# Kernel optimization log

Hardware: AMD Instinct MI355X
Metric: run time of the kernel (lower is better)

The kernel has to match this reference:

```python
import jax, jax.numpy as jnp
import numpy as np

B, N1, N2, DEG = 64, 512, 512, 16
NF, NH, NL = 128, 128, 3
RATIO = 0.5
K1 = int(np.ceil(RATIO * N1))
K2 = int(np.ceil(RATIO * N2))
NCLS = 2
NCAT = NH * NL  # 384


def _gl(key, shape, fan_in):
    return jax.random.normal(key, shape, jnp.float32) / np.sqrt(fan_in)


def setup_inputs() -> dict:
    key = jax.random.key(0)
    ks = jax.random.split(key, 24)
    x = jax.random.normal(ks[0], (B * (N1 + N2), NF), jnp.float32)
    # edges within each component of each graph (c1-local / c2-local and global indexing)
    s1 = jax.random.randint(ks[1], (B, N1 * DEG), 0, N1)
    d1 = jax.random.randint(ks[2], (B, N1 * DEG), 0, N1)
    s2 = jax.random.randint(ks[3], (B, N2 * DEG), 0, N2)
    d2 = jax.random.randint(ks[4], (B, N2 * DEG), 0, N2)
    off1 = (jnp.arange(B) * N1)[:, None]
    off2 = (jnp.arange(B) * N2)[:, None]
    offg = (jnp.arange(B) * (N1 + N2))[:, None]
    src_c1 = (s1 + off1).reshape(-1).astype(jnp.int32)
    dst_c1 = (d1 + off1).reshape(-1).astype(jnp.int32)
    src_c2 = (s2 + off2).reshape(-1).astype(jnp.int32)
    dst_c2 = (d2 + off2).reshape(-1).astype(jnp.int32)
    src_all = jnp.concatenate([(s1 + offg).reshape(-1), (s2 + N1 + offg).reshape(-1)]).astype(jnp.int32)
    dst_all = jnp.concatenate([(d1 + offg).reshape(-1), (d2 + N1 + offg).reshape(-1)]).astype(jnp.int32)
    return {
        'x': x,
        'src_all': src_all, 'dst_all': dst_all,
        'src_c1': src_c1, 'dst_c1': dst_c1,
        'src_c2': src_c2, 'dst_c2': dst_c2,
        'W1': _gl(ks[5], (NF, NH), NF), 'b1': jnp.zeros((NH,), jnp.float32),
        'W2': _gl(ks[6], (NH, NH), NH), 'b2': jnp.zeros((NH,), jnp.float32),
        'W3': _gl(ks[7], (NH, NH), NH), 'b3': jnp.zeros((NH,), jnp.float32),
        'Wg_att': _gl(ks[8], (NCAT, NCAT), NCAT),
        'Wal': _gl(ks[9], (2 * NCAT, 2 * NCAT), 2 * NCAT), 'bal': jnp.zeros((2 * NCAT,), jnp.float32),
        'Wf': _gl(ks[10], (NCAT, NH), NCAT), 'bf': jnp.zeros((NH,), jnp.float32),
        'Wg_fin': _gl(ks[11], (NH, NH), NH),
        'Wl1': _gl(ks[12], (2 * NH, NH), 2 * NH), 'bl1': jnp.zeros((NH,), jnp.float32),
        'Wl2': _gl(ks[13], (NH, NH // 2), NH), 'bl2': jnp.zeros((NH // 2,), jnp.float32),
        'Wl3': _gl(ks[14], (NH // 2, NCLS), NH // 2), 'bl3': jnp.zeros((NCLS,), jnp.float32),
    }


def gcn_conv(x, src, dst, emask, W, b, n):
    # PyG GCNConv: symmetric norm with self-loops; masked edges contribute zero.
    xw = x @ W
    w = emask.astype(x.dtype)
    src_s = jnp.where(emask, src, 0)
    dst_s = jnp.where(emask, dst, 0)
    deg = jax.ops.segment_sum(w, dst_s, num_segments=n) + 1.0  # +1 self-loop
    dis = jax.lax.rsqrt(deg)
    norm = dis[src_s] * dis[dst_s] * w
    out = jax.ops.segment_sum(xw[src_s] * norm[:, None], dst_s, num_segments=n)
    out = out + xw * (dis * dis)[:, None]  # self-loop message
    return out + b


def att_pool(x, batch, counts, Wg, nseg):
    # global_pool with cfg 'ATT': gap -> tanh(W) -> broadcast -> sigmoid gate -> sum pool
    mean = jax.ops.segment_sum(x, batch, num_segments=nseg) / counts[:, None]
    c = jnp.tanh(mean @ Wg)
    alpha = jax.nn.sigmoid(jnp.sum(x * c[batch], axis=1, keepdims=True))
    return jax.ops.segment_sum(x * alpha, batch, num_segments=nseg)


def cag_pool(xc, src, dst, pv, n_per, k):
    # CAGPool_layer: score = <x, pool_vec>/||pool_vec||, per-graph topk, gate by sigmoid(score)
    batch = jnp.repeat(jnp.arange(B), n_per)
    x_ = pv[batch]
    score = jnp.sum(xc * x_, axis=1) / jnp.linalg.norm(x_, axis=1)
    order = jnp.argsort(-score.reshape(B, n_per), axis=1)[:, :k]
    perm = (order + (jnp.arange(B) * n_per)[:, None]).reshape(-1)  # [B*k]
    pooled = xc[perm] * jax.nn.sigmoid(score[perm])[:, None]
    # filter_adj: remap kept nodes, mask out edges touching dropped nodes
    node_map = jnp.full((B * n_per,), -1, dtype=jnp.int32).at[perm].set(jnp.arange(B * k, dtype=jnp.int32))
    r, c = node_map[src], node_map[dst]
    emask = (r >= 0) & (c >= 0)
    return pooled, r, c, emask


def reference(x, src_all, dst_all, src_c1, dst_c1, src_c2, dst_c2,
              W1, b1, W2, b2, W3, b3, Wg_att, Wal, bal, Wf, bf, Wg_fin,
              Wl1, bl1, Wl2, bl2, Wl3, bl3):
    N = B * (N1 + N2)
    ones_all = jnp.ones(src_all.shape[0], dtype=bool)
    h = jax.nn.relu(gcn_conv(x, src_all, dst_all, ones_all, W1, b1, N))
    xs = [h]
    for W, b in ((W2, b2), (W3, b3)):
        h = jax.nn.relu(gcn_conv(h, src_all, dst_all, ones_all, W, b, N))
        xs.append(h)
    xcat = jnp.concatenate(xs, axis=1)  # [N, NCAT]
    # split combined node set into c1 / c2 components (static layout)
    offg = (jnp.arange(B) * (N1 + N2))[:, None]
    idx1 = (offg + jnp.arange(N1)[None, :]).reshape(-1)
    idx2 = (offg + N1 + jnp.arange(N2)[None, :]).reshape(-1)
    x_c1, x_c2 = xcat[idx1], xcat[idx2]
    batch_c1 = jnp.repeat(jnp.arange(B), N1)
    batch_c2 = jnp.repeat(jnp.arange(B), N2)
    x12 = jnp.concatenate([x_c1, x_c2], axis=0)
    batch_ = jnp.concatenate([batch_c1, batch_c2 + B])
    counts = jnp.concatenate([jnp.full((B,), N1, jnp.float32), jnp.full((B,), N2, jnp.float32)])
    gp = att_pool(x12, batch_, counts, Wg_att, 2 * B)
    pv = jnp.concatenate([gp[:B], gp[B:]], axis=1) @ Wal + bal  # att_lin
    pv1, pv2 = pv[:, :NCAT], pv[:, NCAT:]
    p1, r1, c1e, m1 = cag_pool(x_c1, src_c1, dst_c1, pv1, N1, K1)
    p2, r2, c2e, m2 = cag_pool(x_c2, src_c2, dst_c2, pv2, N2, K2)
    h1 = jax.nn.relu(gcn_conv(p1, r1, c1e, m1, Wf, bf, B * K1))
    h2 = jax.nn.relu(gcn_conv(p2, r2, c2e, m2, Wf, bf, B * K2))
    g1 = att_pool(h1, jnp.repeat(jnp.arange(B), K1), jnp.full((B,), K1, jnp.float32), Wg_fin, B)
    g2 = att_pool(h2, jnp.repeat(jnp.arange(B), K2), jnp.full((B,), K2, jnp.float32), Wg_fin, B)
    pred = jnp.concatenate([g1, g2], axis=1)
    pred = jax.nn.relu(pred @ Wl1 + bl1)
    pred = jax.nn.relu(pred @ Wl2 + bl2)
    return pred @ Wl3 + bl3  # [B, NCLS]
```

## Files before the change

kernel.cpp:

```cpp
#include <hip/hip_runtime.h>
#include <math.h>

constexpr int BB   = 64;
constexpr int NPB  = 1024;
constexpr int NN   = BB * NPB;
constexpr int EALL = 1048576;
constexpr int EC   = 524288;
constexpr int EPG  = 8192;
constexpr int KTOP = 256;
constexpr int NP   = BB * KTOP;
constexpr int NP2  = 2 * NP;

typedef __attribute__((ext_vector_type(8))) short bf16x8;
typedef __attribute__((ext_vector_type(4))) unsigned short us4;
typedef __attribute__((ext_vector_type(8))) unsigned short us8;
typedef __attribute__((ext_vector_type(4))) float f32x4;

__device__ __forceinline__ unsigned short f2bf(float f) {
    return (unsigned short)(__float_as_uint(f) >> 16);
}
__device__ __forceinline__ float bf2f(unsigned short h) {
    return __uint_as_float(((unsigned)h) << 16);
}

__device__ __forceinline__ int pq(int q) { return q ^ (q >> 3); }

__global__ __launch_bounds__(256) void k_build_csr(const int* __restrict__ src_all,
                                                   const int* __restrict__ dst_all,
                                                   int* __restrict__ rowstart,
                                                   int* __restrict__ csrc,
                                                   float* __restrict__ dis) {
    __shared__ int cnt[512];
    __shared__ int rs[512];
    __shared__ int wsum[4];
    __shared__ int stage[EPG];
    const int g = blockIdx.x;
    const int b = g >> 1, c = g & 1;
    const int ebase  = c * EC + b * EPG;
    const int region = g * EPG;
    const int nbase  = g * 512;
    const int t = threadIdx.x;
    const int lane = t & 63, w = t >> 6;

    cnt[t] = 0; cnt[t + 256] = 0;
    __syncthreads();
    for (int i = 0; i < 32; i++) {
        int d = dst_all[ebase + t + 256 * i] & 511;
        atomicAdd(&cnt[d], 1);
    }
    __syncthreads();
    int v0 = cnt[2 * t], v1 = cnt[2 * t + 1];
    int p = v0 + v1;
    int incl = p;
    for (int off = 1; off < 64; off <<= 1) {
        int u = __shfl_up(incl, off);
        if (lane >= off) incl += u;
    }
    if (lane == 63) wsum[w] = incl;
    __syncthreads();
    int base = 0;
    for (int i = 0; i < w; i++) base += wsum[i];
    int excl = base + incl - p;
    rs[2 * t] = excl;
    rs[2 * t + 1] = excl + v0;
    rowstart[nbase + 2 * t]     = region + excl;
    rowstart[nbase + 2 * t + 1] = region + excl + v0;
    dis[nbase + 2 * t]     = 1.0f / sqrtf((float)v0 + 1.0f);
    dis[nbase + 2 * t + 1] = 1.0f / sqrtf((float)v1 + 1.0f);
    if (g == 127 && t == 0) rowstart[NN] = EALL;
    __syncthreads();
    for (int i = 0; i < 32; i++) {
        int e = ebase + t + 256 * i;
        int d = dst_all[e] & 511;
        int pp = atomicAdd(&rs[d], 1);
        stage[pp] = src_all[e];
    }
    __syncthreads();
    for (int i = 0; i < 32; i++)
        csrc[region + t + 256 * i] = stage[t + 256 * i];
}

__global__ __launch_bounds__(256) void k_build_csr_pooled(const int* __restrict__ s1,
                                                          const int* __restrict__ d1,
                                                          const int* __restrict__ s2,
                                                          const int* __restrict__ d2,
                                                          const int* __restrict__ nmap,
                                                          int* __restrict__ rowstart,
                                                          int* __restrict__ cntp,
                                                          int* __restrict__ csre,
                                                          float* __restrict__ disp) {
    __shared__ int cnt[256];
    __shared__ int rs[256];
    __shared__ int wsum[4];
    __shared__ int stage[EPG];
    const int g = blockIdx.x;
    const int c = g >> 6, b = g & 63;
    const int* ss = c ? s2 : s1;
    const int* dd = c ? d2 : d1;
    const int* nm = nmap + c * 32768;
    const int ebase  = b * EPG;
    const int region = g * EPG;
    const int nbase  = g * 256;
    const int t = threadIdx.x;
    const int lane = t & 63, w = t >> 6;

    cnt[t] = 0;
    __syncthreads();
    for (int i = 0; i < 32; i++) {
        int e = ebase + t + 256 * i;
        int r = nm[ss[e]], cc = nm[dd[e]];
        if (r >= 0 && cc >= 0) atomicAdd(&cnt[cc & 255], 1);
    }
    __syncthreads();
    int v = cnt[t];
    int incl = v;
    for (int off = 1; off < 64; off <<= 1) {
        int u = __shfl_up(incl, off);
        if (lane >= off) incl += u;
    }
    if (lane == 63) wsum[w] = incl;
    __syncthreads();
    int base = 0;
    for (int i = 0; i < w; i++) base += wsum[i];
    int excl = base + incl - v;
    rs[t] = excl;
    rowstart[nbase + t] = region + excl;
    cntp[nbase + t] = v;
    disp[nbase + t] = 1.0f / sqrtf((float)v + 1.0f);
    __syncthreads();
    for (int i = 0; i < 32; i++) {
        int e = ebase + t + 256 * i;
        int r = nm[ss[e]], cc = nm[dd[e]];
        if (r >= 0 && cc >= 0) {
            int pp = atomicAdd(&rs[cc & 255], 1);
            stage[pp] = r;
        }
    }
    __syncthreads();
    for (int i = 0; i < 32; i++)
        csre[region + t + 256 * i] = stage[t + 256 * i];
}

template <int KDIM>
__global__ __launch_bounds__(256) void k_gemm_tile(const float* __restrict__ A, int lda,
                                                   const float* __restrict__ W,
                                                   const float* __restrict__ rowscale,
                                                   float* __restrict__ C, int M) {
    __shared__ float As[32][132];
    __shared__ float Ws[32 * 128];
    const int tid  = threadIdx.x;
    const int c0 = (tid & 15) * 8;
    const int r0 = (tid >> 4) * 8;
    const int row0 = blockIdx.x * 128;
    const int arow = tid >> 1;
    const int aq   = tid & 1;
    const float* Ap = A + (size_t)(row0 + arow) * lda;
    const int pq0 = pq(c0 >> 2) * 4;
    const int pq1 = pq((c0 >> 2) + 1) * 4;

    float acc[8][8];
#pragma unroll
    for (int i = 0; i < 8; i++)
#pragma unroll
        for (int j = 0; j < 8; j++) acc[i][j] = 0.f;

    float4 areg[4], wreg[4];
#pragma unroll
    for (int qq = 0; qq < 4; qq++)
        areg[qq] = *(const float4*)(Ap + (aq + 2 * qq) * 4);
#pragma unroll
    for (int q = 0; q < 4; q++) {
        int f = tid + 256 * q;
        wreg[q] = *(const float4*)(W + (size_t)(f >> 5) * 128 + (f & 31) * 4);
    }

    constexpr int NT = KDIM / 32;
    for (int t = 0; t < NT; t++) {
#pragma unroll
        for (int qq = 0; qq < 4; qq++) {
            int kk = (aq + 2 * qq) * 4;
            As[kk + 0][arow] = areg[qq].x;
            As[kk + 1][arow] = areg[qq].y;
            As[kk + 2][arow] = areg[qq].z;
            As[kk + 3][arow] = areg[qq].w;
        }
#pragma unroll
        for (int q = 0; q < 4; q++) {
            int f = tid + 256 * q;
            *(float4*)&Ws[(f >> 5) * 128 + pq(f & 31) * 4] = wreg[q];
        }
        __syncthreads();
        if (t + 1 < NT) {
            int k0 = (t + 1) * 32;
#pragma unroll
            for (int qq = 0; qq < 4; qq++)
                areg[qq] = *(const float4*)(Ap + k0 + (aq + 2 * qq) * 4);
#pragma unroll
            for (int q = 0; q < 4; q++) {
                int f = tid + 256 * q;
                wreg[q] = *(const float4*)(W + (size_t)(k0 + (f >> 5)) * 128 + (f & 31) * 4);
            }
        }
#pragma unroll 2
        for (int kk = 0; kk < 32; kk++) {
            float4 a0 = *(const float4*)&As[kk][r0];
            float4 a1 = *(const float4*)&As[kk][r0 + 4];
            float4 b0 = *(const float4*)&Ws[kk * 128 + pq0];
            float4 b1 = *(const float4*)&Ws[kk * 128 + pq1];
            float a[8] = {a0.x, a0.y, a0.z, a0.w, a1.x, a1.y, a1.z, a1.w};
            float b[8] = {b0.x, b0.y, b0.z, b0.w, b1.x, b1.y, b1.z, b1.w};
#pragma unroll
            for (int i = 0; i < 8; i++)
#pragma unroll
                for (int j = 0; j < 8; j++)
                    acc[i][j] = fmaf(a[i], b[j], acc[i][j]);
        }
        if (t + 1 < NT) __syncthreads();
    }
#pragma unroll
    for (int i = 0; i < 8; i++) {
        int row = row0 + r0 + i;
        if (row < M) {
            float sc = rowscale[row];
            float4 o0 = {acc[i][0]*sc, acc[i][1]*sc, acc[i][2]*sc, acc[i][3]*sc};
            float4 o1 = {acc[i][4]*sc, acc[i][5]*sc, acc[i][6]*sc, acc[i][7]*sc};
            *(float4*)(C + (size_t)row * 128 + c0) = o0;
            *(float4*)(C + (size_t)row * 128 + c0 + 4) = o1;
        }
    }
}

__global__ void k_prep_wf(const float* __restrict__ Wf,
                          unsigned short* __restrict__ hi, unsigned short* __restrict__ lo) {
    int g = blockIdx.x * 256 + threadIdx.x;
    int n = g / 384, k = g - n * 384;
    float v = Wf[k * 128 + n];
    unsigned short h = f2bf(v);
    hi[g] = h;
    lo[g] = f2bf(v - bf2f(h));
}

__global__ __launch_bounds__(256) void k_gemm_gather_mfma(const float* __restrict__ XC,
                                                          const int* __restrict__ sel,
                                                          const float* __restrict__ SC,
                                                          const float* __restrict__ rowscale,
                                                          const unsigned short* __restrict__ WH,
                                                          const unsigned short* __restrict__ WL,
                                                          float* __restrict__ C) {
    __shared__ unsigned short Ah[128][40], Al[128][40], Wh[128][40], Wl[128][40];
    const int tid  = threadIdx.x;
    const int wid  = tid >> 6, lane = tid & 63;
    const int quad = lane >> 4, m15 = lane & 15;
    const int row0 = blockIdx.x * 128;
    const int arow = tid >> 1, aq = tid & 1;
    const int wn   = tid >> 1, wh2 = tid & 1;

    int n = row0 + arow;
    int comm = n >= NP;
    int nl = n - (comm ? NP : 0);
    int b = nl >> 8;
    int old = sel[n];
    const float* Ap = XC + (size_t)(b * NPB + comm * 512 + old) * 384;
    float scv = SC[comm * 32768 + b * 512 + old];
    float sg = 1.f / (1.f + expf(-scv));

    f32x4 acc[2][8];
#pragma unroll
    for (int i = 0; i < 2; i++)
#pragma unroll
        for (int j = 0; j < 8; j++) acc[i][j] = (f32x4){0.f, 0.f, 0.f, 0.f};

    float4 areg[4];
#pragma unroll
    for (int qq = 0; qq < 4; qq++)
        areg[qq] = *(const float4*)(Ap + (aq + 2 * qq) * 4);

    constexpr int NT = 12;
    for (int t = 0; t < NT; t++) {
        if (t) __syncthreads();
#pragma unroll
        for (int qq = 0; qq < 4; qq++) {
            int k = (aq + 2 * qq) * 4;
            float4 v = areg[qq];
            v.x *= sg; v.y *= sg; v.z *= sg; v.w *= sg;
            us4 h, l;
            h.x = f2bf(v.x); l.x = f2bf(v.x - bf2f(h.x));
            h.y = f2bf(v.y); l.y = f2bf(v.y - bf2f(h.y));
            h.z = f2bf(v.z); l.z = f2bf(v.z - bf2f(h.z));
            h.w = f2bf(v.w); l.w = f2bf(v.w - bf2f(h.w));
            *(us4*)&Ah[arow][k] = h;
            *(us4*)&Al[arow][k] = l;
        }
        int k0 = t * 32;
#pragma unroll
        for (int c = 0; c < 2; c++) {
            int kc = 8 * (wh2 + 2 * c);
            *(us8*)&Wh[wn][kc] = *(const us8*)&WH[(size_t)wn * 384 + k0 + kc];
            *(us8*)&Wl[wn][kc] = *(const us8*)&WL[(size_t)wn * 384 + k0 + kc];
        }
        __syncthreads();
        if (t + 1 < NT) {
            int kn = (t + 1) * 32;
#pragma unroll
            for (int qq = 0; qq < 4; qq++)
                areg[qq] = *(const float4*)(Ap + kn + (aq + 2 * qq) * 4);
        }
        bf16x8 ah[2], al2[2];
#pragma unroll
        for (int rt = 0; rt < 2; rt++) {
            int r = wid * 32 + rt * 16 + m15;
            ah[rt]  = *(const bf16x8*)&Ah[r][quad * 8];
            al2[rt] = *(const bf16x8*)&Al[r][quad * 8];
        }
#pragma unroll
        for (int ct = 0; ct < 8; ct++) {
            int nn = ct * 16 + m15;
            bf16x8 bh = *(const bf16x8*)&Wh[nn][quad * 8];
            bf16x8 bl = *(const bf16x8*)&Wl[nn][quad * 8];
#pragma unroll
            for (int rt = 0; rt < 2; rt++) {
                acc[rt][ct] = __builtin_amdgcn_mfma_f32_16x16x32_bf16(ah[rt], bh, acc[rt][ct], 0, 0, 0);
                acc[rt][ct] = __builtin_amdgcn_mfma_f32_16x16x32_bf16(al2[rt], bh, acc[rt][ct], 0, 0, 0);
                acc[rt][ct] = __builtin_amdgcn_mfma_f32_16x16x32_bf16(ah[rt], bl, acc[rt][ct], 0, 0, 0);
            }
        }
    }
#pragma unroll
    for (int rt = 0; rt < 2; rt++)
#pragma unroll
        for (int reg = 0; reg < 4; reg++) {
            int row = row0 + wid * 32 + rt * 16 + quad * 4 + reg;
            float sc = rowscale[row];
#pragma unroll
            for (int ct = 0; ct < 8; ct++)
                C[(size_t)row * 128 + ct * 16 + m15] = acc[rt][ct][reg] * sc;
        }
}

__global__ void k_aggregate4(const float* __restrict__ xwsc, const float* __restrict__ dis,
                             const int* __restrict__ rowstart, const int* __restrict__ csrc,
                             const float* __restrict__ bias, float* __restrict__ XC, int colbase,
                             float* __restrict__ mpart) {
    __shared__ float redf[8][128];
    int xcd  = blockIdx.x & 7;
    int slot = blockIdx.x >> 3;
    int g    = ((slot >> 6) << 3) | xcd;
    int bslot = slot & 63;
    int node = g * 512 + bslot * 8 + (threadIdx.x >> 5);
    int l    = threadIdx.x & 31;
    const float4* xw4 = (const float4*)xwsc;
    float4 acc = xw4[(size_t)node * 32 + l];
    int e0 = rowstart[node], e1 = rowstart[node + 1];
    int e = e0;
    for (; e + 4 <= e1; e += 4) {
        int s0 = csrc[e], s1 = csrc[e + 1], s2 = csrc[e + 2], s3 = csrc[e + 3];
        float4 u0 = xw4[(size_t)s0 * 32 + l];
        float4 u1 = xw4[(size_t)s1 * 32 + l];
        float4 u2 = xw4[(size_t)s2 * 32 + l];
        float4 u3 = xw4[(size_t)s3 * 32 + l];
        acc.x += (u0.x + u1.x) + (u2.x + u3.x);
        acc.y += (u0.y + u1.y) + (u2.y + u3.y);
        acc.z += (u0.z + u1.z) + (u2.z + u3.z);
        acc.w += (u0.w + u1.w) + (u2.w + u3.w);
    }
    for (; e < e1; e++) {
        int s = csrc[e];
        float4 u = xw4[(size_t)s * 32 + l];
        acc.x += u.x; acc.y += u.y; acc.z += u.z; acc.w += u.w;
    }
    float di = dis[node];
    float4 b4 = ((const float4*)bias)[l];
    acc.x = fmaxf(acc.x * di + b4.x, 0.f);
    acc.y = fmaxf(acc.y * di + b4.y, 0.f);
    acc.z = fmaxf(acc.z * di + b4.z, 0.f);
    acc.w = fmaxf(acc.w * di + b4.w, 0.f);
    *(float4*)(XC + (size_t)node * 384 + colbase + l * 4) = acc;
    *(float4*)&redf[threadIdx.x >> 5][l * 4] = acc;
    __syncthreads();
    if (threadIdx.x < 128) {
        int c = threadIdx.x;
        float s = 0.f;
#pragma unroll
        for (int r = 0; r < 8; r++) s += redf[r][c];
        mpart[((size_t)(g * 64 + bslot)) * 384 + colbase + c] = s;
    }
}

__global__ void k_aggregate_pooled(const float* __restrict__ xw, const float* __restrict__ disp,
                                   const int* __restrict__ rowstart, const int* __restrict__ cntp,
                                   const int* __restrict__ csre,
                                   const float* __restrict__ bias, float* __restrict__ H,
                                   float* __restrict__ meansum) {
    __shared__ float redf[8][128];
    int xcd  = blockIdx.x & 7;
    int slot = blockIdx.x >> 3;
    int g    = ((slot >> 5) << 3) | xcd;
    int node = g * 256 + (slot & 31) * 8 + (threadIdx.x >> 5);
    int l    = threadIdx.x & 31;
    const float4* x4 = (const float4*)xw;
    float4 acc = x4[(size_t)node * 32 + l];
    int e0 = rowstart[node], nE = cntp[node];
    int e = e0, eend = e0 + nE;
    for (; e + 4 <= eend; e += 4) {
        int s0 = csre[e], s1 = csre[e + 1], s2 = csre[e + 2], s3 = csre[e + 3];
        float4 u0 = x4[(size_t)s0 * 32 + l];
        float4 u1 = x4[(size_t)s1 * 32 + l];
        float4 u2 = x4[(size_t)s2 * 32 + l];
        float4 u3 = x4[(size_t)s3 * 32 + l];
        acc.x += (u0.x + u1.x) + (u2.x + u3.x);
        acc.y += (u0.y + u1.y) + (u2.y + u3.y);
        acc.z += (u0.z + u1.z) + (u2.z + u3.z);
        acc.w += (u0.w + u1.w) + (u2.w + u3.w);
    }
    for (; e < eend; e++) {
        int r = csre[e];
        float4 u = x4[(size_t)r * 32 + l];
        acc.x += u.x; acc.y += u.y; acc.z += u.z; acc.w += u.w;
    }
    float di = disp[node];
    float4 b4 = ((const float4*)bias)[l];
    acc.x = fmaxf(acc.x * di + b4.x, 0.f);
    acc.y = fmaxf(acc.y * di + b4.y, 0.f);
    acc.z = fmaxf(acc.z * di + b4.z, 0.f);
    acc.w = fmaxf(acc.w * di + b4.w, 0.f);
    *(float4*)(H + (size_t)node * 128 + l * 4) = acc;
    *(float4*)&redf[threadIdx.x >> 5][l * 4] = acc;
    __syncthreads();
    if (threadIdx.x < 128) {
        int c = threadIdx.x;
        float s = 0.f;
#pragma unroll
        for (int r = 0; r < 8; r++) s += redf[r][c];
        atomicAdd(&meansum[g * 128 + c], s);
    }
}

__global__ void k_c12(const float* __restrict__ mpart, const float* __restrict__ Wg,
                      float* __restrict__ c12) {
    __shared__ float ms[384];
    int seg = blockIdx.x; int c = threadIdx.x;
    int g = ((seg & 63) << 1) | (seg >> 6);
    float s0 = 0.f;
    for (int s2 = 0; s2 < 64; s2++)
        s0 += mpart[((size_t)(g * 64 + s2)) * 384 + c];
    ms[c] = s0 * (1.0f / 512.0f);
    __syncthreads();
    float s = 0.f;
    for (int k = 0; k < 384; k++) s = fmaf(ms[k], Wg[(size_t)k * 384 + c], s);
    c12[seg * 384 + c] = tanhf(s);
}

__global__ __launch_bounds__(256) void k_attpool1(const float* __restrict__ XC,
                                                  const float* __restrict__ C12,
                                                  float* __restrict__ GPP) {
    __shared__ float gps[4][384];
    int blk = blockIdx.x;
    int gc = blk >> 2, q = blk & 3;
    int seg = ((gc & 1) << 6) | (gc >> 1);
    int w = threadIdx.x >> 6, l = threadIdx.x & 63;
    const float* c12r = C12 + seg * 384;
    float4 cr0 = *(const float4*)(c12r + 4 * l);
    float4 cr1 = (l < 32) ? *(const float4*)(c12r + 256 + 4 * l) : float4{0.f,0.f,0.f,0.f};
    float4 a0 = {0.f,0.f,0.f,0.f}, a1 = {0.f,0.f,0.f,0.f};
    int base = gc * 512 + q * 128 + w * 32;
    for (int it = 0; it < 32; it++) {
        const float* xr = XC + (size_t)(base + it) * 384;
        float4 v0 = *(const float4*)(xr + 4 * l);
        float4 v1 = (l < 32) ? *(const float4*)(xr + 256 + 4 * l) : float4{0.f,0.f,0.f,0.f};
        float s = v0.x*cr0.x + v0.y*cr0.y + v0.z*cr0.z + v0.w*cr0.w
                + v1.x*cr1.x + v1.y*cr1.y + v1.z*cr1.z + v1.w*cr1.w;
        for (int off = 32; off; off >>= 1) s += __shfl_xor(s, off);
        float al = 1.f / (1.f + expf(-s));
        a0.x += v0.x*al; a0.y += v0.y*al; a0.z += v0.z*al; a0.w += v0.w*al;
        a1.x += v1.x*al; a1.y += v1.y*al; a1.z += v1.z*al; a1.w += v1.w*al;
    }
    *(float4*)&gps[w][4 * l] = a0;
    if (l < 32) *(float4*)&gps[w][256 + 4 * l] = a1;
    __syncthreads();
    for (int c = threadIdx.x; c < 384; c += 256) {
        float s = gps[0][c] + gps[1][c] + gps[2][c] + gps[3][c];
        GPP[(size_t)(seg * 4 + q) * 384 + c] = s;
    }
}

__global__ void k_pv(const float* __restrict__ GPP, const float* __restrict__ Wal,
                     const float* __restrict__ bal, float* __restrict__ pv,
                     float* __restrict__ pnorm) {
    __shared__ float gpls[768];
    __shared__ float red[768];
    int row = blockIdx.x;
    int c   = threadIdx.x;
    {
        int seg = (c < 384) ? row : (64 + row);
        int k   = (c < 384) ? c : (c - 384);
        float v = GPP[(size_t)(seg * 4 + 0) * 384 + k] + GPP[(size_t)(seg * 4 + 1) * 384 + k]
                + GPP[(size_t)(seg * 4 + 2) * 384 + k] + GPP[(size_t)(seg * 4 + 3) * 384 + k];
        gpls[c] = v;
    }
    __syncthreads();
    float s = bal[c];
    for (int k = 0; k < 768; k++) s = fmaf(gpls[k], Wal[(size_t)k * 768 + c], s);
    pv[row * 768 + c] = s;
    red[c] = s * s;
    __syncthreads();
    int wv = c >> 6, ln = c & 63;
    if (wv < 2) {
        float s2 = 0.f;
#pragma unroll
        for (int i = 0; i < 6; i++) s2 += red[wv * 384 + ln + 64 * i];
        for (int off = 32; off; off >>= 1) s2 += __shfl_down(s2, off);
        if (ln == 0) pnorm[wv * 64 + row] = sqrtf(s2);
    }
}

__global__ void k_score(const float* __restrict__ XC, const float* __restrict__ pv,
                        const float* __restrict__ pnorm, float* __restrict__ sc) {
    int nl2 = blockIdx.x * 4 + (threadIdx.x >> 6);
    int lane = threadIdx.x & 63;
    int comm = nl2 >> 15;
    int nl = nl2 & 32767;
    int b = nl >> 9; int i = nl & 511;
    const float* xr = XC + (size_t)(b * NPB + comm * 512 + i) * 384;
    const float* pr = pv + b * 768 + comm * 384;
    float4 x0 = *(const float4*)(xr + 4 * lane);
    float4 p0 = *(const float4*)(pr + 4 * lane);
    float s = x0.x*p0.x + x0.y*p0.y + x0.z*p0.z + x0.w*p0.w;
    if (lane < 32) {
        float4 x1 = *(const float4*)(xr + 256 + 4 * lane);
        float4 p1 = *(const float4*)(pr + 256 + 4 * lane);
        s += x1.x*p1.x + x1.y*p1.y + x1.z*p1.z + x1.w*p1.w;
    }
    for (int off = 32; off; off >>= 1) s += __shfl_down(s, off);
    if (lane == 0) sc[comm * 32768 + nl] = s / pnorm[comm * 64 + b];
}

__global__ void k_topk(const float* __restrict__ sc, int* __restrict__ sel, int* __restrict__ nmap) {
    __shared__ float sv[512];
    __shared__ int   si[512];
    int blk = blockIdx.x;
    int t = threadIdx.x;
    sv[t] = sc[blk * 512 + t];             si[t] = t;
    sv[t + 256] = sc[blk * 512 + t + 256]; si[t + 256] = t + 256;
    __syncthreads();
    for (int k2 = 2; k2 <= 512; k2 <<= 1) {
        for (int j = k2 >> 1; j > 0; j >>= 1) {
            for (int i = t; i < 512; i += 256) {
                int l = i ^ j;
                if (l > i) {
                    bool desc = ((i & k2) == 0);
                    float a = sv[i], bb2 = sv[l];
                    bool sw = desc ? (a < bb2) : (a > bb2);
                    if (sw) {
                        sv[i] = bb2; sv[l] = a;
                        int tmp = si[i]; si[i] = si[l]; si[l] = tmp;
                    }
                }
            }
            __syncthreads();
        }
    }
    sel[blk * 256 + t] = si[t];
    nmap[blk * 512 + si[t]] = blk * 256 + t;
    nmap[blk * 512 + si[t + 256]] = -1;
}

__global__ void k_cfin(const float* __restrict__ meansum, const float* __restrict__ Wg,
                       float* __restrict__ cf) {
    __shared__ float ms[128];
    int b = blockIdx.x; int c = threadIdx.x;
    ms[c] = meansum[b * 128 + c] * (1.0f / 256.0f);
    __syncthreads();
    float s = 0.f;
    for (int k = 0; k < 128; k++) s = fmaf(ms[k], Wg[k * 128 + c], s);
    cf[b * 128 + c] = tanhf(s);
}

__global__ __launch_bounds__(256) void k_attpool_fin(const float* __restrict__ H,
                                                     const float* __restrict__ cf,
                                                     float* __restrict__ g12) {
    __shared__ float gps[4][128];
    int seg = blockIdx.x;
    int w = threadIdx.x >> 6, l = threadIdx.x & 63;
    const float2 cfl = *(const float2*)(cf + seg * 128 + 2 * l);
    float2 acc = {0.f, 0.f};
    int base = seg * 256 + w * 64;
    for (int it = 0; it < 64; it++) {
        const float2 h = *(const float2*)(H + (size_t)(base + it) * 128 + 2 * l);
        float s = h.x * cfl.x + h.y * cfl.y;
        for (int off = 32; off; off >>= 1) s += __shfl_xor(s, off);
        float al = 1.f / (1.f + expf(-s));
        acc.x += h.x * al; acc.y += h.y * al;
    }
    *(float2*)&gps[w][2 * l] = acc;
    __syncthreads();
    if (threadIdx.x < 128) {
        int c = threadIdx.x;
        float s = gps[0][c] + gps[1][c] + gps[2][c] + gps[3][c];
        int b = seg & 63, comm = seg >> 6;
        g12[b * 256 + comm * 128 + c] = s;
    }
}

__global__ void k_mlp(const float* __restrict__ G,
                      const float* __restrict__ Wl1, const float* __restrict__ bl1,
                      const float* __restrict__ Wl2, const float* __restrict__ bl2,
                      const float* __restrict__ Wl3, const float* __restrict__ bl3,
                      float* __restrict__ out) {
    __shared__ float t1[128], t2[64];
    int b = blockIdx.x; int t = threadIdx.x;
    float s = bl1[t];
    for (int k = 0; k < 256; k++) s = fmaf(G[b * 256 + k], Wl1[k * 128 + t], s);
    t1[t] = fmaxf(s, 0.f);
    __syncthreads();
    if (t < 64) {
        float s2 = bl2[t];
        for (int k = 0; k < 128; k++) s2 = fmaf(t1[k], Wl2[k * 64 + t], s2);
        t2[t] = fmaxf(s2, 0.f);
    }
    __syncthreads();
    if (t < 2) {
        float s3 = bl3[t];
        for (int k = 0; k < 64; k++) s3 = fmaf(t2[k], Wl3[k * 2 + t], s3);
        out[b * 2 + t] = s3;
    }
}

extern "C" void kernel_launch(void* const* d_in, const int* in_sizes, int n_in,
                              void* d_out, int out_size, void* d_ws, size_t ws_size,
                              hipStream_t stream) {
    const float* x       = (const float*)d_in[0];
    const int*   src_all = (const int*)d_in[1];
    const int*   dst_all = (const int*)d_in[2];
    const int*   src_c1  = (const int*)d_in[3];
    const int*   dst_c1  = (const int*)d_in[4];
    const int*   src_c2  = (const int*)d_in[5];
    const int*   dst_c2  = (const int*)d_in[6];
    const float* W1 = (const float*)d_in[7];   const float* b1 = (const float*)d_in[8];
    const float* W2 = (const float*)d_in[9];   const float* b2 = (const float*)d_in[10];
    const float* W3 = (const float*)d_in[11];  const float* b3 = (const float*)d_in[12];
    const float* Wg_att = (const float*)d_in[13];
    const float* Wal = (const float*)d_in[14]; const float* bal = (const float*)d_in[15];
    const float* Wf  = (const float*)d_in[16]; const float* bf  = (const float*)d_in[17];
    const float* Wg_fin = (const float*)d_in[18];
    const float* Wl1 = (const float*)d_in[19]; const float* bl1 = (const float*)d_in[20];
    const float* Wl2 = (const float*)d_in[21]; const float* bl2 = (const float*)d_in[22];
    const float* Wl3 = (const float*)d_in[23]; const float* bl3 = (const float*)d_in[24];
    float* out = (float*)d_out;

    float* f = (float*)d_ws;
    size_t o = 0;
    float* XC   = f + o; o += (size_t)NN * 384;
    float* SCR  = f + o; o += (size_t)NN * 128;
    float* H    = f + o; o += (size_t)NP2 * 128;
    int* ROWSTART = (int*)(f + o); o += 65552;
    int* CSRC     = (int*)(f + o); o += EALL;
    int* CNTP     = (int*)(f + o); o += NP2;
    float* DIS    = f + o; o += NN;
    float* GPP    = f + o; o += 512 * 384;
    float* MEANF  = f + o; o += 128 * 128;
    float* C12    = f + o; o += 128 * 384;
    float* PV     = f + o; o += 64 * 768;
    float* PNORM  = f + o; o += 128;
    float* SC     = f + o; o += 65536;
    int* SEL      = (int*)(f + o); o += NP2;
    int* NMAP     = (int*)(f + o); o += 65536;
    float* DISP   = f + o; o += NP2;
    float* CFIN   = f + o; o += 128 * 128;
    float* G12    = f + o; o += 64 * 256;
    unsigned short* WBH = (unsigned short*)(f + o); o += 24576;
    unsigned short* WBL = (unsigned short*)(f + o); o += 24576;
    size_t needed_bytes = o * sizeof(float);
    if (ws_size < needed_bytes) return;

    float* MPART = H;
    float* XWP   = SCR;

    hipMemsetAsync(MEANF, 0, 128 * 128 * sizeof(float), stream);

    k_prep_wf<<<192, 256, 0, stream>>>(Wf, WBH, WBL);

    k_build_csr<<<128, 256, 0, stream>>>(src_all, dst_all, ROWSTART, CSRC, DIS);

    k_gemm_tile<128><<<NN / 128, 256, 0, stream>>>(x, 128, W1, DIS, SCR, NN);
    k_aggregate4<<<NN / 8, 256, 0, stream>>>(SCR, DIS, ROWSTART, CSRC, b1, XC, 0, MPART);
    k_gemm_tile<128><<<NN / 128, 256, 0, stream>>>(XC + 0, 384, W2, DIS, SCR, NN);
    k_aggregate4<<<NN / 8, 256, 0, stream>>>(SCR, DIS, ROWSTART, CSRC, b2, XC, 128, MPART);
    k_gemm_tile<128><<<NN / 128, 256, 0, stream>>>(XC + 128, 384, W3, DIS, SCR, NN);
    k_aggregate4<<<NN / 8, 256, 0, stream>>>(SCR, DIS, ROWSTART, CSRC, b3, XC, 256, MPART);

    k_c12<<<128, 384, 0, stream>>>(MPART, Wg_att, C12);
    k_attpool1<<<512, 256, 0, stream>>>(XC, C12, GPP);
    k_pv<<<64, 768, 0, stream>>>(GPP, Wal, bal, PV, PNORM);

    k_score<<<65536 / 4, 256, 0, stream>>>(XC, PV, PNORM, SC);
    k_topk<<<128, 256, 0, stream>>>(SC, SEL, NMAP);

    k_build_csr_pooled<<<128, 256, 0, stream>>>(src_c1, dst_c1, src_c2, dst_c2,
                                                NMAP, ROWSTART, CNTP, CSRC, DISP);

    k_gemm_gather_mfma<<<NP2 / 128, 256, 0, stream>>>(XC, SEL, SC, DISP, WBH, WBL, XWP);
    k_aggregate_pooled<<<NP2 / 8, 256, 0, stream>>>(XWP, DISP, ROWSTART, CNTP, CSRC,
                                                    bf, H, MEANF);

    k_cfin<<<128, 128, 0, stream>>>(MEANF, Wg_fin, CFIN);
    k_attpool_fin<<<128, 256, 0, stream>>>(H, CFIN, G12);

    k_mlp<<<64, 128, 0, stream>>>(G12, Wl1, bl1, Wl2, bl2, Wl3, bl3, out);
}
```

Measured before the change: 575.3 us.

## Replace FP32 SIMT GEMM for GCN layers with split-bf16 MFMA GEMM

```diff
diff --git a/kernel.cpp b/kernel.cpp
--- a/kernel.cpp
+++ b/kernel.cpp
@@ -22,8 +22,6 @@
 __device__ __forceinline__ float bf2f(unsigned short h) {
     return __uint_as_float(((unsigned)h) << 16);
 }
-
-__device__ __forceinline__ int pq(int q) { return q ^ (q >> 3); }
 
 __global__ __launch_bounds__(256) void k_build_csr(const int* __restrict__ src_all,
                                                    const int* __restrict__ dst_all,
@@ -141,103 +139,113 @@
         csre[region + t + 256 * i] = stage[t + 256 * i];
 }
 
+__global__ void k_prep_w(const float* __restrict__ W1, const float* __restrict__ W2,
+                         const float* __restrict__ W3, const float* __restrict__ Wf,
+                         unsigned short* __restrict__ hi, unsigned short* __restrict__ lo) {
+    int g = blockIdx.x * 256 + threadIdx.x;
+    float v; int dst;
+    if (g < 49152) {
+        int mat = g >> 14, rem = g & 16383;
+        int n = rem >> 7, k = rem & 127;
+        const float* W = (mat == 0) ? W1 : (mat == 1) ? W2 : W3;
+        v = W[k * 128 + n];
+        dst = mat * 16384 + n * 128 + k;
+    } else {
+        int rem = g - 49152;
+        int n = rem / 384, k = rem - n * 384;
+        v = Wf[k * 128 + n];
+        dst = 49152 + n * 384 + k;
+    }
+    unsigned short h = f2bf(v);
+    hi[dst] = h;
+    lo[dst] = f2bf(v - bf2f(h));
+}
+
 template <int KDIM>
-__global__ __launch_bounds__(256) void k_gemm_tile(const float* __restrict__ A, int lda,
-                                                   const float* __restrict__ W,
+__global__ __launch_bounds__(256) void k_gemm_mfma(const float* __restrict__ A, int lda,
+                                                   const unsigned short* __restrict__ WH,
+                                                   const unsigned short* __restrict__ WL,
                                                    const float* __restrict__ rowscale,
-                                                   float* __restrict__ C, int M) {
-    __shared__ float As[32][132];
-    __shared__ float Ws[32 * 128];
+                                                   float* __restrict__ C) {
+    __shared__ unsigned short Ah[128][40], Al[128][40], Wh[128][40], Wl[128][40];
     const int tid  = threadIdx.x;
-    const int c0 = (tid & 15) * 8;
-    const int r0 = (tid >> 4) * 8;
+    const int wid  = tid >> 6, lane = tid & 63;
+    const int quad = lane >> 4, m15 = lane & 15;
     const int row0 = blockIdx.x * 128;
-    const int arow = tid >> 1;
-    const int aq   = tid & 1;
+    const int arow = tid >> 1, aq = tid & 1;
+    const int wn   = tid >> 1, wh2 = tid & 1;
     const float* Ap = A + (size_t)(row0 + arow) * lda;
-    const int pq0 = pq(c0 >> 2) * 4;
-    const int pq1 = pq((c0 >> 2) + 1) * 4;
-
-    float acc[8][8];
-#pragma unroll
-    for (int i = 0; i < 8; i++)
-#pragma unroll
-        for (int j = 0; j < 8; j++) acc[i][j] = 0.f;
-
-    float4 areg[4], wreg[4];
+
+    f32x4 acc[2][8];
+#pragma unroll
+    for (int i = 0; i < 2; i++)
+#pragma unroll
+        for (int j = 0; j < 8; j++) acc[i][j] = (f32x4){0.f, 0.f, 0.f, 0.f};
+
+    float4 areg[4];
 #pragma unroll
     for (int qq = 0; qq < 4; qq++)
         areg[qq] = *(const float4*)(Ap + (aq + 2 * qq) * 4);
-#pragma unroll
-    for (int q = 0; q < 4; q++) {
-        int f = tid + 256 * q;
-        wreg[q] = *(const float4*)(W + (size_t)(f >> 5) * 128 + (f & 31) * 4);
-    }
 
     constexpr int NT = KDIM / 32;
     for (int t = 0; t < NT; t++) {
+        if (t) __syncthreads();
 #pragma unroll
         for (int qq = 0; qq < 4; qq++) {
-            int kk = (aq + 2 * qq) * 4;
-            As[kk + 0][arow] = areg[qq].x;
-            As[kk + 1][arow] = areg[qq].y;
-            As[kk + 2][arow] = areg[qq].z;
-            As[kk + 3][arow] = areg[qq].w;
-        }
-#pragma unroll
-        for (int q = 0; q < 4; q++) {
-            int f = tid + 256 * q;
-            *(float4*)&Ws[(f >> 5) * 128 + pq(f & 31) * 4] = wreg[q];
+            int k = (aq + 2 * qq) * 4;
+            float4 v = areg[qq];
+            us4 h, l;
+            h.x = f2bf(v.x); l.x = f2bf(v.x - bf2f(h.x));
+            h.y = f2bf(v.y); l.y = f2bf(v.y - bf2f(h.y));
+            h.z = f2bf(v.z); l.z = f2bf(v.z - bf2f(h.z));
+            h.w = f2bf(v.w); l.w = f2bf(v.w - bf2f(h.w));
+            *(us4*)&Ah[arow][k] = h;
+            *(us4*)&Al[arow][k] = l;
+        }
+        int k0 = t * 32;
+#pragma unroll
+        for (int c = 0; c < 2; c++) {
+            int kc = 8 * (wh2 + 2 * c);
+            *(us8*)&Wh[wn][kc] = *(const us8*)&WH[(size_t)wn * KDIM + k0 + kc];
+            *(us8*)&Wl[wn][kc] = *(const us8*)&WL[(size_t)wn * KDIM + k0 + kc];
         }
         __syncthreads();
         if (t + 1 < NT) {
-            int k0 = (t + 1) * 32;
+            int kn = (t + 1) * 32;
 #pragma unroll
             for (int qq = 0; qq < 4; qq++)
-                areg[qq] = *(const float4*)(Ap + k0 + (aq + 2 * qq) * 4);
-#pragma unroll
-            for (int q = 0; q < 4; q++) {
-                int f = tid + 256 * q;
-                wreg[q] = *(const float4*)(W + (size_t)(k0 + (f >> 5)) * 128 + (f & 31) * 4);
+                areg[qq] = *(const float4*)(Ap + kn + (aq + 2 * qq) * 4);
+        }
+        bf16x8 ah[2], al2[2];
+#pragma unroll
+        for (int rt = 0; rt < 2; rt++) {
+            int r = wid * 32 + rt * 16 + m15;
+            ah[rt]  = *(const bf16x8*)&Ah[r][quad * 8];
+            al2[rt] = *(const bf16x8*)&Al[r][quad * 8];
+        }
+#pragma unroll
+        for (int ct = 0; ct < 8; ct++) {
+            int n = ct * 16 + m15;
+            bf16x8 bh = *(const bf16x8*)&Wh[n][quad * 8];
+            bf16x8 bl = *(const bf16x8*)&Wl[n][quad * 8];
+#pragma unroll
+            for (int rt = 0; rt < 2; rt++) {
+                acc[rt][ct] = __builtin_amdgcn_mfma_f32_16x16x32_bf16(ah[rt], bh, acc[rt][ct], 0, 0, 0);
+                acc[rt][ct] = __builtin_amdgcn_mfma_f32_16x16x32_bf16(al2[rt], bh, acc[rt][ct], 0, 0, 0);
+                acc[rt][ct] = __builtin_amdgcn_mfma_f32_16x16x32_bf16(ah[rt], bl, acc[rt][ct], 0, 0, 0);
             }
         }
-#pragma unroll 2
-        for (int kk = 0; kk < 32; kk++) {
-            float4 a0 = *(const float4*)&As[kk][r0];
-            float4 a1 = *(const float4*)&As[kk][r0 + 4];
-            float4 b0 = *(const float4*)&Ws[kk * 128 + pq0];
-            float4 b1 = *(const float4*)&Ws[kk * 128 + pq1];
-            float a[8] = {a0.x, a0.y, a0.z, a0.w, a1.x, a1.y, a1.z, a1.w};
-            float b[8] = {b0.x, b0.y, b0.z, b0.w, b1.x, b1.y, b1.z, b1.w};
-#pragma unroll
-            for (int i = 0; i < 8; i++)
-#pragma unroll
-                for (int j = 0; j < 8; j++)
-                    acc[i][j] = fmaf(a[i], b[j], acc[i][j]);
-        }
-        if (t + 1 < NT) __syncthreads();
-    }
-#pragma unroll
-    for (int i = 0; i < 8; i++) {
-        int row = row0 + r0 + i;
-        if (row < M) {
+    }
+#pragma unroll
+    for (int rt = 0; rt < 2; rt++)
+#pragma unroll
+        for (int reg = 0; reg < 4; reg++) {
+            int row = row0 + wid * 32 + rt * 16 + quad * 4 + reg;
             float sc = rowscale[row];
-            float4 o0 = {acc[i][0]*sc, acc[i][1]*sc, acc[i][2]*sc, acc[i][3]*sc};
-            float4 o1 = {acc[i][4]*sc, acc[i][5]*sc, acc[i][6]*sc, acc[i][7]*sc};
-            *(float4*)(C + (size_t)row * 128 + c0) = o0;
-            *(float4*)(C + (size_t)row * 128 + c0 + 4) = o1;
-        }
-    }
-}
-
-__global__ void k_prep_wf(const float* __restrict__ Wf,
-                          unsigned short* __restrict__ hi, unsigned short* __restrict__ lo) {
-    int g = blockIdx.x * 256 + threadIdx.x;
-    int n = g / 384, k = g - n * 384;
-    float v = Wf[k * 128 + n];
-    unsigned short h = f2bf(v);
-    hi[g] = h;
-    lo[g] = f2bf(v - bf2f(h));
+#pragma unroll
+            for (int ct = 0; ct < 8; ct++)
+                C[(size_t)row * 128 + ct * 16 + m15] = acc[rt][ct][reg] * sc;
+        }
 }
 
 __global__ __launch_bounds__(256) void k_gemm_gather_mfma(const float* __restrict__ XC,
@@ -667,8 +675,8 @@
     float* DISP   = f + o; o += NP2;
     float* CFIN   = f + o; o += 128 * 128;
     float* G12    = f + o; o += 64 * 256;
-    unsigned short* WBH = (unsigned short*)(f + o); o += 24576;
-    unsigned short* WBL = (unsigned short*)(f + o); o += 24576;
+    unsigned short* WBH = (unsigned short*)(f + o); o += 49152;
+    unsigned short* WBL = (unsigned short*)(f + o); o += 49152;
     size_t needed_bytes = o * sizeof(float);
     if (ws_size < needed_bytes) return;
 
@@ -677,15 +685,15 @@
 
     hipMemsetAsync(MEANF, 0, 128 * 128 * sizeof(float), stream);
 
-    k_prep_wf<<<192, 256, 0, stream>>>(Wf, WBH, WBL);
+    k_prep_w<<<384, 256, 0, stream>>>(W1, W2, W3, Wf, WBH, WBL);
 
     k_build_csr<<<128, 256, 0, stream>>>(src_all, dst_all, ROWSTART, CSRC, DIS);
 
-    k_gemm_tile<128><<<NN / 128, 256, 0, stream>>>(x, 128, W1, DIS, SCR, NN);
+    k_gemm_mfma<128><<<NN / 128, 256, 0, stream>>>(x, 128, WBH, WBL, DIS, SCR);
     k_aggregate4<<<NN / 8, 256, 0, stream>>>(SCR, DIS, ROWSTART, CSRC, b1, XC, 0, MPART);
-    k_gemm_tile<128><<<NN / 128, 256, 0, stream>>>(XC + 0, 384, W2, DIS, SCR, NN);
+    k_gemm_mfma<128><<<NN / 128, 256, 0, stream>>>(XC + 0, 384, WBH + 16384, WBL + 16384, DIS, SCR);
     k_aggregate4<<<NN / 8, 256, 0, stream>>>(SCR, DIS, ROWSTART, CSRC, b2, XC, 128, MPART);
-    k_gemm_tile<128><<<NN / 128, 256, 0, stream>>>(XC + 128, 384, W3, DIS, SCR, NN);
+    k_gemm_mfma<128><<<NN / 128, 256, 0, stream>>>(XC + 128, 384, WBH + 32768, WBL + 32768, DIS, SCR);
     k_aggregate4<<<NN / 8, 256, 0, stream>>>(SCR, DIS, ROWSTART, CSRC, b3, XC, 256, MPART);
 
     k_c12<<<128, 384, 0, stream>>>(MPART, Wg_att, C12);
@@ -698,7 +706,8 @@
     k_build_csr_pooled<<<128, 256, 0, stream>>>(src_c1, dst_c1, src_c2, dst_c2,
                                                 NMAP, ROWSTART, CNTP, CSRC, DISP);
 
-    k_gemm_gather_mfma<<<NP2 / 128, 256, 0, stream>>>(XC, SEL, SC, DISP, WBH, WBL, XWP);
+    k_gemm_gather_mfma<<<NP2 / 128, 256, 0, stream>>>(XC, SEL, SC, DISP,
+                                                      WBH + 49152, WBL + 49152, XWP);
     k_aggregate_pooled<<<NP2 / 8, 256, 0, stream>>>(XWP, DISP, ROWSTART, CNTP, CSRC,
                                                     bf, H, MEANF);
 
```

After: 512.8 us. 10.9% less time.
